# Kernel optimization log

Hardware: AMD Instinct MI355X
Metric: run time of the kernel (lower is better)

Reference implementation:

```python
import jax, jax.numpy as jnp
import numpy as np

CF_ITERS = 5
CF_K = 0.02
DECAY = [0.9, 0.93, 0.85, 0.97, 0.88, 0.94]
N_CHAMBERS = 6
RES_DIM = 100
B = 262144

COUPLING = np.array([
    [0.0, -0.3, 0.6, 0.4, -0.2, 0.3],
    [-0.3, 0.0, -0.5, -0.7, 0.6, 0.4],
    [0.6, -0.5, 0.0, 0.3, -0.3, 0.2],
    [0.4, -0.7, 0.3, 0.0, -0.4, 0.5],
    [-0.2, 0.6, -0.3, -0.4, 0.0, 0.3],
    [0.3, 0.4, 0.2, 0.5, 0.3, 0.0]], dtype=np.float32)


def _init_linear(key, c, fan_out, fan_in):
    kw, kb = jax.random.split(key)
    bound = 1.0 / np.sqrt(fan_in)
    W = jax.random.uniform(kw, (c, fan_out, fan_in), jnp.float32, -bound, bound)
    b = jax.random.uniform(kb, (c, fan_out), jnp.float32, -bound, bound)
    return W, b


def setup_inputs() -> dict:
    key = jax.random.key(0)
    ks = jax.random.split(key, 5)
    res = jax.random.normal(ks[0], (B, RES_DIM), jnp.float32)
    W1, b1 = _init_linear(ks[1], N_CHAMBERS, 128, RES_DIM)
    W2, b2 = _init_linear(ks[2], N_CHAMBERS, 64, 128)
    W3, b3 = _init_linear(ks[3], N_CHAMBERS, 32, 64)
    W4, b4 = _init_linear(ks[4], N_CHAMBERS, 1, 32)
    coupling = jnp.asarray(COUPLING)
    return {"res": res, "W1": W1, "b1": b1, "W2": W2, "b2": b2,
            "W3": W3, "b3": b3, "W4": W4, "b4": b4, "coupling": coupling}


def reference(res, W1, b1, W2, b2, W3, b3, W4, b4, coupling):
    silu = jax.nn.silu
    # batched 6 per-chamber MLPs: [B, C, hidden]
    h = silu(jnp.einsum('bd,chd->bch', res, W1) + b1)      # [B,6,128]
    h = silu(jnp.einsum('bch,coh->bco', h, W2) + b2)       # [B,6,64]
    h = silu(jnp.einsum('bco,cpo->bcp', h, W3) + b3)       # [B,6,32]
    raw = (jnp.einsum('bcp,cqp->bcq', h, W4) + b4)[..., 0]  # [B,6]
    act = jax.nn.sigmoid(raw)
    decay = jnp.asarray(DECAY, dtype=jnp.float32)
    for _ in range(CF_ITERS):
        act = act * decay
        # infl[b,i,j] = CF_K * sin(act[b,j] - act[b,i])
        infl = CF_K * jnp.sin(act[:, None, :] - act[:, :, None])  # [B,6,6]
        act = act + jnp.sum(infl * coupling[None], axis=2)
        act = jnp.clip(act, 0.0, 1.0)
    return (act, raw)
```

## Files before the change

kernel.cpp:

```cpp
#include <hip/hip_runtime.h>


typedef unsigned int u32;
typedef unsigned short u16;
typedef __attribute__((ext_vector_type(8))) short bf16x8;
typedef __attribute__((ext_vector_type(4))) float f32x4;

#define RES_DIM 100
#define NCH 6
#define FRAGS_PER_CH 52
#define NFRAG (NCH*FRAGS_PER_CH)
#define WS_BYTES ((size_t)NFRAG*2048)

#define MFMA16 __builtin_amdgcn_mfma_f32_16x16x32_bf16

union FragU { bf16x8 v; u32 u[4]; uint4 q; };

__device__ __forceinline__ void split2(float f0, float f1, u32 &hp, u32 &lp){
    u32 u0 = __float_as_uint(f0), u1 = __float_as_uint(f1);
    u32 h0 = (u0 + 0x7fffu + ((u0>>16)&1u)) & 0xffff0000u;
    u32 h1 = (u1 + 0x7fffu + ((u1>>16)&1u)) & 0xffff0000u;
    hp = (h0 >> 16) | h1;
    float l0 = f0 - __uint_as_float(h0);
    float l1 = f1 - __uint_as_float(h1);
    lp = (__float_as_uint(l0) >> 16) | (__float_as_uint(l1) & 0xffff0000u);
}

__device__ __forceinline__ float silu1(float x){
    return x * __builtin_amdgcn_rcpf(1.f + __expf(-x));
}
__device__ __forceinline__ f32x4 silu4(f32x4 v){
    f32x4 r; r[0]=silu1(v[0]); r[1]=silu1(v[1]); r[2]=silu1(v[2]); r[3]=silu1(v[3]); return r;
}
__device__ __forceinline__ float sin_rev(float x){ return __builtin_amdgcn_sinf(x*0.15915494309189535f); }

__device__ __forceinline__ void load_frag(const u32* __restrict__ wsb, int frag, int lane,
                                          bf16x8 &h, bf16x8 &l){
    const uint4* p = (const uint4*)(wsb + ((size_t)frag << 9) + (lane << 3));
    FragU H, L; H.q = p[0]; L.q = p[1];
    h = H.v; l = L.v;
}

__device__ __forceinline__ f32x4 triple(f32x4 acc, bf16x8 ah, bf16x8 al, bf16x8 bh, bf16x8 bl){
    acc = MFMA16(ah, bh, acc, 0, 0, 0);
    acc = MFMA16(al, bh, acc, 0, 0, 0);
    acc = MFMA16(ah, bl, acc, 0, 0, 0);
    return acc;
}

__global__ void __launch_bounds__(64) prep_kernel(
    const float* __restrict__ W1, const float* __restrict__ W2,
    const float* __restrict__ W3, u32* __restrict__ ws)
{
    const int f = blockIdx.x;
    const int lane = threadIdx.x;
    const int c = f / FRAGS_PER_CH, r = f % FRAGS_PER_CH;
    const int n15 = lane & 15, quad = lane >> 4;
    float vals[8];
    if (r < 32) {
        int n = r >> 2, k = r & 3;
        const float* wp = W1 + (size_t)c*128*RES_DIM + (size_t)(n*16 + n15)*RES_DIM;
        #pragma unroll
        for (int j=0;j<8;j++){
            int kk = k*32 + quad*8 + j;
            vals[j] = (kk < RES_DIM) ? wp[kk] : 0.f;
        }
    } else if (r < 48) {
        int rr = r - 32; int n = rr >> 2, k = rr & 3;
        const float* wp = W2 + (size_t)c*64*128 + (size_t)(n*16 + n15)*128;
        #pragma unroll
        for (int j=0;j<8;j++) vals[j] = wp[k*32 + quad*8 + j];
    } else {
        int rr = r - 48; int n = rr >> 1, k = rr & 1;
        const float* wp = W3 + (size_t)c*32*64 + (size_t)(n*16 + n15)*64;
        #pragma unroll
        for (int j=0;j<8;j++) vals[j] = wp[k*32 + quad*8 + j];
    }
    u32 hp[4], lp[4];
    #pragma unroll
    for (int i=0;i<4;i++) split2(vals[2*i], vals[2*i+1], hp[i], lp[i]);
    u32* dst = ws + ((size_t)f << 9) + (lane << 3);
    *(uint4*)(dst)     = make_uint4(hp[0],hp[1],hp[2],hp[3]);
    *(uint4*)(dst + 4) = make_uint4(lp[0],lp[1],lp[2],lp[3]);
}

#define TB_STRIDE 36
#define TB_SIZE (32*TB_STRIDE)

__global__ void __launch_bounds__(256, 2) chambers_mfma(
    const float* __restrict__ res, const u32* __restrict__ wsb,
    const float* __restrict__ b1, const float* __restrict__ b2,
    const float* __restrict__ b3, const float* __restrict__ W4,
    const float* __restrict__ b4, const float* __restrict__ Cpl,
    float* __restrict__ out, int nsamp)
{
    __shared__ __align__(16) float tb[4][TB_SIZE];
    __shared__ float rawld[4*32*7];

    const int tid  = threadIdx.x;
    const int w    = tid >> 6, lane = tid & 63;
    const int n15  = lane & 15, quad = lane >> 4;
    const int m_base = (blockIdx.x * 4 + w) * 32;

    bf16x8 rh[2][4], rl[2][4];
    #pragma unroll
    for (int mt=0; mt<2; mt++){
        const float* row = res + (size_t)(m_base + mt*16 + n15) * RES_DIM;
        #pragma unroll
        for (int ks=0; ks<4; ks++){
            float v[8];
            if (ks < 3){
                float4 A = *(const float4*)(row + ks*32 + quad*8);
                float4 B = *(const float4*)(row + ks*32 + quad*8 + 4);
                v[0]=A.x; v[1]=A.y; v[2]=A.z; v[3]=A.w;
                v[4]=B.x; v[5]=B.y; v[6]=B.z; v[7]=B.w;
            } else {
                float4 A = make_float4(0.f,0.f,0.f,0.f);
                if (quad == 0) A = *(const float4*)(row + 96);
                v[0]=A.x; v[1]=A.y; v[2]=A.z; v[3]=A.w;
                v[4]=0.f; v[5]=0.f; v[6]=0.f; v[7]=0.f;
            }
            FragU H, L;
            #pragma unroll
            for (int i=0;i<4;i++) split2(v[2*i], v[2*i+1], H.u[i], L.u[i]);
            rh[mt][ks]=H.v; rl[mt][ks]=L.v;
        }
    }

    for (int c=0; c<NCH; c++){
        const float* b1c = b1 + c*128;
        const float* b2c = b2 + c*64;
        const float* b3c = b3 + c*32;
        const int fbase = c*FRAGS_PER_CH;

        f32x4 c2[2][4];
        #pragma unroll
        for (int mt=0; mt<2; mt++)
            #pragma unroll
            for (int nt=0; nt<4; nt++){
                float bb = b2c[nt*16 + n15];
                f32x4 t = {bb,bb,bb,bb}; c2[mt][nt] = t;
            }

        for (int kk=0; kk<4; kk++){
            f32x4 d1[2][2];
            #pragma unroll
            for (int pp=0; pp<2; pp++){
                int p = kk*2 + pp;
                float bb = b1c[p*16 + n15];
                f32x4 a0 = {bb,bb,bb,bb}, a1 = a0;
                #pragma unroll
                for (int ks=0; ks<4; ks++){
                    bf16x8 bh, bl; load_frag(wsb, fbase + p*4 + ks, lane, bh, bl);
                    a0 = triple(a0, rh[0][ks], rl[0][ks], bh, bl);
                    a1 = triple(a1, rh[1][ks], rl[1][ks], bh, bl);
                }
                d1[0][pp] = silu4(a0);
                d1[1][pp] = silu4(a1);
            }
            __syncthreads();
            #pragma unroll
            for (int mt=0; mt<2; mt++)
                #pragma unroll
                for (int pp=0; pp<2; pp++)
                    #pragma unroll
                    for (int r=0; r<4; r++)
                        tb[w][(mt*16 + quad*4 + r)*TB_STRIDE + pp*16 + n15] = d1[mt][pp][r];
            __syncthreads();
            bf16x8 a2h[2], a2l[2];
            #pragma unroll
            for (int mt=0; mt<2; mt++){
                const float* qp = &tb[w][(mt*16 + n15)*TB_STRIDE + quad*8];
                float4 A = *(const float4*)qp;
                float4 B = *(const float4*)(qp + 4);
                FragU H, L;
                split2(A.x, A.y, H.u[0], L.u[0]);
                split2(A.z, A.w, H.u[1], L.u[1]);
                split2(B.x, B.y, H.u[2], L.u[2]);
                split2(B.z, B.w, H.u[3], L.u[3]);
                a2h[mt]=H.v; a2l[mt]=L.v;
            }
            #pragma unroll
            for (int nt=0; nt<4; nt++){
                bf16x8 bh, bl; load_frag(wsb, fbase + 32 + nt*4 + kk, lane, bh, bl);
                c2[0][nt] = triple(c2[0][nt], a2h[0], a2l[0], bh, bl);
                c2[1][nt] = triple(c2[1][nt], a2h[1], a2l[1], bh, bl);
            }
        }
        #pragma unroll
        for (int mt=0; mt<2; mt++)
            #pragma unroll
            for (int nt=0; nt<4; nt++) c2[mt][nt] = silu4(c2[mt][nt]);

        f32x4 c3[2][2];
        #pragma unroll
        for (int mt=0; mt<2; mt++)
            #pragma unroll
            for (int nt=0; nt<2; nt++){
                float bb = b3c[nt*16 + n15];
                f32x4 t = {bb,bb,bb,bb}; c3[mt][nt] = t;
            }
        for (int k3=0; k3<2; k3++){
            __syncthreads();
            #pragma unroll
            for (int mt=0; mt<2; mt++)
                #pragma unroll
                for (int q2=0; q2<2; q2++)
                    #pragma unroll
                    for (int r=0; r<4; r++)
                        tb[w][(mt*16 + quad*4 + r)*TB_STRIDE + q2*16 + n15] = c2[mt][2*k3+q2][r];
            __syncthreads();
            bf16x8 a3h[2], a3l[2];
            #pragma unroll
            for (int mt=0; mt<2; mt++){
                const float* qp = &tb[w][(mt*16 + n15)*TB_STRIDE + quad*8];
                float4 A = *(const float4*)qp;
                float4 B = *(const float4*)(qp + 4);
                FragU H, L;
                split2(A.x, A.y, H.u[0], L.u[0]);
                split2(A.z, A.w, H.u[1], L.u[1]);
                split2(B.x, B.y, H.u[2], L.u[2]);
                split2(B.z, B.w, H.u[3], L.u[3]);
                a3h[mt]=H.v; a3l[mt]=L.v;
            }
            #pragma unroll
            for (int nt=0; nt<2; nt++){
                bf16x8 bh, bl; load_frag(wsb, fbase + 48 + nt*2 + k3, lane, bh, bl);
                c3[0][nt] = triple(c3[0][nt], a3h[0], a3l[0], bh, bl);
                c3[1][nt] = triple(c3[1][nt], a3h[1], a3l[1], bh, bl);
            }
        }
        #pragma unroll
        for (int mt=0; mt<2; mt++)
            #pragma unroll
            for (int nt=0; nt<2; nt++) c3[mt][nt] = silu4(c3[mt][nt]);

        float w4a = W4[c*32 + n15];
        float w4b = W4[c*32 + 16 + n15];
        float bb4 = b4[c];
        #pragma unroll
        for (int mt=0; mt<2; mt++){
            float t0 = c3[mt][0][0]*w4a + c3[mt][1][0]*w4b;
            float t1 = c3[mt][0][1]*w4a + c3[mt][1][1]*w4b;
            float t2 = c3[mt][0][2]*w4a + c3[mt][1][2]*w4b;
            float t3 = c3[mt][0][3]*w4a + c3[mt][1][3]*w4b;
            #pragma unroll
            for (int off=1; off<16; off<<=1){
                t0 += __shfl_xor(t0, off, 64);
                t1 += __shfl_xor(t1, off, 64);
                t2 += __shfl_xor(t2, off, 64);
                t3 += __shfl_xor(t3, off, 64);
            }
            if (n15 == 0){
                int mb = w*32 + mt*16 + quad*4;
                rawld[(mb+0)*7 + c] = t0 + bb4;
                rawld[(mb+1)*7 + c] = t1 + bb4;
                rawld[(mb+2)*7 + c] = t2 + bb4;
                rawld[(mb+3)*7 + c] = t3 + bb4;
            }
        }
    }
    __syncthreads();

    const int m = lane & 31;
    float rw[6], a[6];
    #pragma unroll
    for (int j=0;j<6;j++){
        rw[j] = rawld[(w*32 + m)*7 + j];
        a[j]  = __builtin_amdgcn_rcpf(1.f + __expf(-rw[j]));
    }
    const float dec[6] = {0.9f,0.93f,0.85f,0.97f,0.88f,0.94f};
    float C[6][6];
    #pragma unroll
    for (int i=0;i<6;i++)
        #pragma unroll
        for (int j=0;j<6;j++) C[i][j] = Cpl[i*6+j];
    #pragma unroll
    for (int it=0; it<5; it++){
        #pragma unroll
        for (int j=0;j<6;j++) a[j] *= dec[j];
        float nz[6];
        #pragma unroll
        for (int i=0;i<6;i++){
            float sum = 0.f;
            #pragma unroll
            for (int j=0;j<6;j++) sum += sin_rev(a[j]-a[i]) * C[i][j];
            nz[i] = a[i] + 0.02f*sum;
        }
        #pragma unroll
        for (int i=0;i<6;i++) a[i] = fminf(fmaxf(nz[i],0.f),1.f);
    }
    if (lane < 32){
        size_t s = (size_t)m_base + m;
        #pragma unroll
        for (int j=0;j<6;j++) out[s*6 + j] = a[j];
        size_t rb = (size_t)nsamp*6 + s*6;
        #pragma unroll
        for (int j=0;j<6;j++) out[rb + j] = rw[j];
    }
}

__global__ void __launch_bounds__(256, 2) chambers_fb(
    const float* __restrict__ res, const float* __restrict__ W1, const float* __restrict__ b1,
    const float* __restrict__ W2, const float* __restrict__ b2,
    const float* __restrict__ W3, const float* __restrict__ b3,
    const float* __restrict__ W4, const float* __restrict__ b4,
    const float* __restrict__ Cpl, float* __restrict__ out, int nsamp)
{
    __shared__ float w2t[128*64];
    __shared__ float h3buf[256][33];
    __shared__ float rawbuf[256][7];
    const int tid = threadIdx.x;
    const long long s = (long long)blockIdx.x * 256 + tid;
    float rf[RES_DIM];
    {
        const float4* rp = (const float4*)(res + s*RES_DIM);
        #pragma unroll
        for (int i=0;i<25;i++){
            float4 v = rp[i];
            rf[4*i+0]=v.x; rf[4*i+1]=v.y; rf[4*i+2]=v.z; rf[4*i+3]=v.w;
        }
    }
    for (int c=0;c<6;c++){
        __syncthreads();
        {
            const float* w2c = W2 + c*64*128;
            for (int k=tid; k<64*128; k+=256){
                int o = k >> 7, u = k & 127;
                w2t[u*64 + o] = w2c[k];
            }
        }
        __syncthreads();
        const float* w1c = W1 + c*128*RES_DIM;
        const float* b1c = b1 + c*128;
        const float* b2c = b2 + c*64;
        float h2a[64];
        #pragma unroll
        for (int o=0;o<64;o++) h2a[o] = b2c[o];
        for (int u=0; u<128; u+=2){
            const float4* wa = (const float4*)(w1c + u*RES_DIM);
            const float4* wb = wa + 25;
            float a0=0.f,a1=0.f,a2=0.f,a3=0.f;
            #pragma unroll
            for (int i=0;i<25;i++){
                float4 va=wa[i], vb=wb[i];
                a0 = fmaf(va.x, rf[4*i+0], a0); a0 = fmaf(va.y, rf[4*i+1], a0);
                a2 = fmaf(va.z, rf[4*i+2], a2); a2 = fmaf(va.w, rf[4*i+3], a2);
                a1 = fmaf(vb.x, rf[4*i+0], a1); a1 = fmaf(vb.y, rf[4*i+1], a1);
                a3 = fmaf(vb.z, rf[4*i+2], a3); a3 = fmaf(vb.w, rf[4*i+3], a3);
            }
            float hh0 = silu1(a0+a2+b1c[u]);
            float hh1 = silu1(a1+a3+b1c[u+1]);
            const float* wr0 = &w2t[u*64];
            const float* wr1 = &w2t[(u+1)*64];
            #pragma unroll
            for (int o=0;o<64;o+=4){
                float4 va = *(const float4*)(wr0+o);
                float4 vb = *(const float4*)(wr1+o);
                h2a[o+0] = fmaf(va.x, hh0, fmaf(vb.x, hh1, h2a[o+0]));
                h2a[o+1] = fmaf(va.y, hh0, fmaf(vb.y, hh1, h2a[o+1]));
                h2a[o+2] = fmaf(va.z, hh0, fmaf(vb.z, hh1, h2a[o+2]));
                h2a[o+3] = fmaf(va.w, hh0, fmaf(vb.w, hh1, h2a[o+3]));
            }
        }
        #pragma unroll
        for (int o=0;o<64;o++) h2a[o] = silu1(h2a[o]);
        {
            const float* w3c = W3 + c*32*64;
            const float* b3c = b3 + c*32;
            for (int p=0; p<32; p+=2){
                const float4* wa = (const float4*)(w3c + p*64);
                const float4* wb = wa + 16;
                float a0=0.f,a1=0.f,a2=0.f,a3=0.f;
                #pragma unroll
                for (int k=0;k<16;k++){
                    float4 va=wa[k], vb=wb[k];
                    a0 = fmaf(va.x, h2a[4*k+0], a0); a0 = fmaf(va.y, h2a[4*k+1], a0);
                    a2 = fmaf(va.z, h2a[4*k+2], a2); a2 = fmaf(va.w, h2a[4*k+3], a2);
                    a1 = fmaf(vb.x, h2a[4*k+0], a1); a1 = fmaf(vb.y, h2a[4*k+1], a1);
                    a3 = fmaf(vb.z, h2a[4*k+2], a3); a3 = fmaf(vb.w, h2a[4*k+3], a3);
                }
                h3buf[tid][p]   = silu1(a0+a2+b3c[p]);
                h3buf[tid][p+1] = silu1(a1+a3+b3c[p+1]);
            }
        }
        {
            const float4* w4p = (const float4*)(W4 + c*32);
            float a0=0.f, a1=0.f;
            #pragma unroll
            for (int k=0;k<8;k++){
                float4 v = w4p[k];
                a0 = fmaf(v.x, h3buf[tid][4*k+0], a0);
                a1 = fmaf(v.y, h3buf[tid][4*k+1], a1);
                a0 = fmaf(v.z, h3buf[tid][4*k+2], a0);
                a1 = fmaf(v.w, h3buf[tid][4*k+3], a1);
            }
            rawbuf[tid][c] = a0+a1+b4[c];
        }
    }
    float a[6], rw[6];
    #pragma unroll
    for (int j=0;j<6;j++){ rw[j]=rawbuf[tid][j]; a[j]=__builtin_amdgcn_rcpf(1.f+__expf(-rw[j])); }
    const float dec[6] = {0.9f,0.93f,0.85f,0.97f,0.88f,0.94f};
    float C[6][6];
    #pragma unroll
    for (int i=0;i<6;i++)
        #pragma unroll
        for (int j=0;j<6;j++) C[i][j]=Cpl[i*6+j];
    #pragma unroll
    for (int it=0; it<5; it++){
        #pragma unroll
        for (int j=0;j<6;j++) a[j]*=dec[j];
        float nz[6];
        #pragma unroll
        for (int i=0;i<6;i++){
            float sum=0.f;
            #pragma unroll
            for (int j=0;j<6;j++) sum += sin_rev(a[j]-a[i]) * C[i][j];
            nz[i]=a[i]+0.02f*sum;
        }
        #pragma unroll
        for (int i=0;i<6;i++) a[i]=fminf(fmaxf(nz[i],0.f),1.f);
    }
    long long ob = s*6;
    #pragma unroll
    for (int j=0;j<6;j++) out[ob+j] = a[j];
    long long rb = (long long)nsamp*6 + ob;
    #pragma unroll
    for (int j=0;j<6;j++) out[rb+j] = rw[j];
}

extern "C" void kernel_launch(void* const* d_in, const int* in_sizes, int n_in,
                              void* d_out, int out_size, void* d_ws, size_t ws_size,
                              hipStream_t stream) {
    const float* res = (const float*)d_in[0];
    const float* W1  = (const float*)d_in[1];
    const float* b1  = (const float*)d_in[2];
    const float* W2  = (const float*)d_in[3];
    const float* b2  = (const float*)d_in[4];
    const float* W3  = (const float*)d_in[5];
    const float* b3  = (const float*)d_in[6];
    const float* W4  = (const float*)d_in[7];
    const float* b4  = (const float*)d_in[8];
    const float* Cpl = (const float*)d_in[9];
    float* out = (float*)d_out;
    int nsamp = in_sizes[0] / RES_DIM;

    if (ws_size >= WS_BYTES) {
        u32* ws = (u32*)d_ws;
        prep_kernel<<<NFRAG, 64, 0, stream>>>(W1, W2, W3, ws);
        chambers_mfma<<<nsamp/128, 256, 0, stream>>>(res, ws, b1, b2, b3, W4, b4, Cpl, out, nsamp);
    } else {
        chambers_fb<<<nsamp/256, 256, 0, stream>>>(res, W1, b1, W2, b2, W3, b3, W4, b4, Cpl, out, nsamp);
    }
}
```

Measured before the change: 505.9 us.

## Replace block barriers with wave-local fences, split MFMA chains, prefetch weights

Each wave only reads its own slice of the shared staging buffer, so workgroup-wide __syncthreads barriers are replaced by __threadfence_block around the write/read of the per-wave tile. The layer-1 triple-bf16 accumulation is split into three independent MFMA accumulator chains to cut dependency latency. Layer-2/3 weight fragments are loaded ahead of the LDS round-trip so their latency can overlap. Risks include correctness if the fence does not order LDS accesses across lanes within a wave, plus higher register pressure.

Result: faster. 441.6 us (-12.7%).

```diff
diff --git a/kernel.cpp b/kernel.cpp
--- a/kernel.cpp
+++ b/kernel.cpp
@@ -2,7 +2,6 @@
 
 
 typedef unsigned int u32;
-typedef unsigned short u16;
 typedef __attribute__((ext_vector_type(8))) short bf16x8;
 typedef __attribute__((ext_vector_type(4))) float f32x4;
 
@@ -143,30 +142,36 @@
             }
 
         for (int kk=0; kk<4; kk++){
-            f32x4 d1[2][2];
+            bf16x8 w2h[4], w2l[4];
+            #pragma unroll
+            for (int nt=0; nt<4; nt++) load_frag(wsb, fbase + 32 + nt*4 + kk, lane, w2h[nt], w2l[nt]);
+
             #pragma unroll
             for (int pp=0; pp<2; pp++){
                 int p = kk*2 + pp;
                 float bb = b1c[p*16 + n15];
-                f32x4 a0 = {bb,bb,bb,bb}, a1 = a0;
+                f32x4 z = {0.f,0.f,0.f,0.f};
+                f32x4 A0h = {bb,bb,bb,bb}, A0u = z, A0v = z;
+                f32x4 A1h = A0h,           A1u = z, A1v = z;
                 #pragma unroll
                 for (int ks=0; ks<4; ks++){
                     bf16x8 bh, bl; load_frag(wsb, fbase + p*4 + ks, lane, bh, bl);
-                    a0 = triple(a0, rh[0][ks], rl[0][ks], bh, bl);
-                    a1 = triple(a1, rh[1][ks], rl[1][ks], bh, bl);
+                    A0h = MFMA16(rh[0][ks], bh, A0h, 0,0,0);
+                    A1h = MFMA16(rh[1][ks], bh, A1h, 0,0,0);
+                    A0u = MFMA16(rl[0][ks], bh, A0u, 0,0,0);
+                    A1u = MFMA16(rl[1][ks], bh, A1u, 0,0,0);
+                    A0v = MFMA16(rh[0][ks], bl, A0v, 0,0,0);
+                    A1v = MFMA16(rh[1][ks], bl, A1v, 0,0,0);
                 }
-                d1[0][pp] = silu4(a0);
-                d1[1][pp] = silu4(a1);
-            }
-            __syncthreads();
-            #pragma unroll
-            for (int mt=0; mt<2; mt++)
+                f32x4 s0 = silu4((A0h + A0u) + A0v);
+                f32x4 s1 = silu4((A1h + A1u) + A1v);
                 #pragma unroll
-                for (int pp=0; pp<2; pp++)
-                    #pragma unroll
-                    for (int r=0; r<4; r++)
-                        tb[w][(mt*16 + quad*4 + r)*TB_STRIDE + pp*16 + n15] = d1[mt][pp][r];
-            __syncthreads();
+                for (int r=0; r<4; r++){
+                    tb[w][(quad*4 + r)*TB_STRIDE      + pp*16 + n15] = s0[r];
+                    tb[w][(16 + quad*4 + r)*TB_STRIDE + pp*16 + n15] = s1[r];
+                }
+            }
+            __threadfence_block();
             bf16x8 a2h[2], a2l[2];
             #pragma unroll
             for (int mt=0; mt<2; mt++){
@@ -180,11 +185,11 @@
                 split2(B.z, B.w, H.u[3], L.u[3]);
                 a2h[mt]=H.v; a2l[mt]=L.v;
             }
+            __threadfence_block();
             #pragma unroll
             for (int nt=0; nt<4; nt++){
-                bf16x8 bh, bl; load_frag(wsb, fbase + 32 + nt*4 + kk, lane, bh, bl);
-                c2[0][nt] = triple(c2[0][nt], a2h[0], a2l[0], bh, bl);
-                c2[1][nt] = triple(c2[1][nt], a2h[1], a2l[1], bh, bl);
+                c2[0][nt] = triple(c2[0][nt], a2h[0], a2l[0], w2h[nt], w2l[nt]);
+                c2[1][nt] = triple(c2[1][nt], a2h[1], a2l[1], w2h[nt], w2l[nt]);
             }
         }
         #pragma unroll
@@ -201,7 +206,9 @@
                 f32x4 t = {bb,bb,bb,bb}; c3[mt][nt] = t;
             }
         for (int k3=0; k3<2; k3++){
-            __syncthreads();
+            bf16x8 w3h[2], w3l[2];
+            #pragma unroll
+            for (int nt=0; nt<2; nt++) load_frag(wsb, fbase + 48 + nt*2 + k3, lane, w3h[nt], w3l[nt]);
             #pragma unroll
             for (int mt=0; mt<2; mt++)
                 #pragma unroll
@@ -209,7 +216,7 @@
                     #pragma unroll
                     for (int r=0; r<4; r++)
                         tb[w][(mt*16 + quad*4 + r)*TB_STRIDE + q2*16 + n15] = c2[mt][2*k3+q2][r];
-            __syncthreads();
+            __threadfence_block();
             bf16x8 a3h[2], a3l[2];
             #pragma unroll
             for (int mt=0; mt<2; mt++){
@@ -223,11 +230,11 @@
                 split2(B.z, B.w, H.u[3], L.u[3]);
                 a3h[mt]=H.v; a3l[mt]=L.v;
             }
+            __threadfence_block();
             #pragma unroll
             for (int nt=0; nt<2; nt++){
-                bf16x8 bh, bl; load_frag(wsb, fbase + 48 + nt*2 + k3, lane, bh, bl);
-                c3[0][nt] = triple(c3[0][nt], a3h[0], a3l[0], bh, bl);
-                c3[1][nt] = triple(c3[1][nt], a3h[1], a3l[1], bh, bl);
+                c3[0][nt] = triple(c3[0][nt], a3h[0], a3l[0], w3h[nt], w3l[nt]);
+                c3[1][nt] = triple(c3[1][nt], a3h[1], a3l[1], w3h[nt], w3l[nt]);
             }
         }
         #pragma unroll
@@ -260,7 +267,7 @@
             }
         }
     }
-    __syncthreads();
+    __threadfence_block();
 
     const int m = lane & 31;
     float rw[6], a[6];
```
